# Performance work log

Hardware: AMD Instinct MI355X
Metric: run time of the kernel (lower is better)

## Reference

```python
import jax, jax.numpy as jnp
import numpy as np

B, N, E = 64, 512, 8192          # graphs, nodes per graph, edges per graph
F_IN, H, C = 128, 128, 10        # in features, hidden, classes
K1, K2 = 256, 128                # dense pool cluster counts: ceil(.5*N), ceil(.5*K1)
EPS = 1e-15


def setup_inputs():
    key = jax.random.key(0)
    keys = jax.random.split(key, 32)
    it = iter(keys)
    def w(shape, fan_in):
        return jax.random.normal(next(it), shape, jnp.float32) / np.sqrt(fan_in)
    x = jax.random.normal(next(it), (B * N, F_IN), jnp.float32)
    src_l = jax.random.randint(next(it), (B, E), 0, N)
    dst_l = jax.random.randint(next(it), (B, E), 0, N)
    off = (jnp.arange(B) * N)[:, None]
    src = (src_l + off).reshape(-1).astype(jnp.int32)
    dst = (dst_l + off).reshape(-1).astype(jnp.int32)
    return dict(
        x=x, src=src, dst=dst,
        conv0_wr=w((F_IN, H), F_IN), conv0_wroot=w((F_IN, H), F_IN), conv0_b=jnp.zeros((H,), jnp.float32),
        sconv2_wr=w((H, H), H), sconv2_wroot=w((H, H), H), sconv2_b=jnp.zeros((H,), jnp.float32),
        sconv3_wr=w((H, H), H), sconv3_wroot=w((H, H), H), sconv3_b=jnp.zeros((H,), jnp.float32),
        sage1_wr=w((H, H), H), sage1_wroot=w((H, H), H), sage1_b=jnp.zeros((H,), jnp.float32),
        sage2_wr=w((H, H), H), sage2_wroot=w((H, H), H), sage2_b=jnp.zeros((H,), jnp.float32),
        pool0_w=w((H, K1), H), pool0_b=jnp.zeros((K1,), jnp.float32),
        pool1_w=w((H, K2), H), pool1_b=jnp.zeros((K2,), jnp.float32),
        p1=w((H,), H), p2=w((H,), H), p3=w((H,), H),
        lin1_1_w=w((2 * H, H), 2 * H), lin1_1_b=jnp.zeros((H,), jnp.float32),
        lin1_w=w((H, H), H), lin1_b=jnp.zeros((H,), jnp.float32),
        lin2_w=w((2 * H, C), 2 * H), lin2_b=jnp.zeros((C,), jnp.float32),
    )


def _graph_conv(x, src, dst, emask, wr, wroot, b, n):
    # PyG GraphConv: lin_rel(sum_j x_j) + lin_root(x_i); invalid edges masked to 0.
    msg = x[src] * emask[:, None]
    agg = jax.ops.segment_sum(msg, dst, num_segments=n)
    return agg @ wr + x @ wroot + b


def _topk_pool(x, score_w, src, dst, emask, n_per_graph, k):
    # TopK pooling (MPoolS): score = x.w/||w||, keep top ratio*n per graph, gate by tanh(score).
    score = x @ score_w / (jnp.linalg.norm(score_w) + 1e-16)
    idx = jax.lax.top_k(score.reshape(B, n_per_graph), k)[1]
    perm = (idx + (jnp.arange(B) * n_per_graph)[:, None]).reshape(-1)
    new_x = x[perm] * jnp.tanh(score[perm])[:, None]
    new_id = jnp.full((B * n_per_graph,), -1, jnp.int32).at[perm].set(
        jnp.arange(B * k, dtype=jnp.int32))
    ns, nd = new_id[src], new_id[dst]
    valid = (ns >= 0) & (nd >= 0) & (emask > 0)
    return new_x, jnp.where(valid, ns, 0), jnp.where(valid, nd, 0), valid.astype(x.dtype)


def _readout(x, k):
    # gmp || gap per graph (nodes are contiguous, k per graph)
    xr = x.reshape(B, k, -1)
    return jnp.concatenate([xr.max(axis=1), xr.mean(axis=1)], axis=-1)


def _dense_sage(x, adj, wr, wroot, b):
    agg = (adj @ x) / jnp.clip(adj.sum(-1, keepdims=True), 1.0, None)
    return agg @ wr + x @ wroot + b


def _dense_mincut_pool(x, adj, s):
    s = jax.nn.softmax(s, axis=-1)
    k = s.shape[-1]
    out = jnp.einsum('bnk,bnf->bkf', s, x)
    out_adj = jnp.einsum('bnk,bnm,bml->bkl', s, adj, s)
    mincut_num = jnp.trace(out_adj, axis1=-2, axis2=-1)
    deg = adj.sum(-1)
    mincut_den = jnp.einsum('bn,bnk,bnk->b', deg, s, s)
    mc = -jnp.mean(mincut_num / (mincut_den + EPS))
    ss = jnp.einsum('bnk,bnl->bkl', s, s)
    ss_n = jnp.linalg.norm(ss, axis=(1, 2), keepdims=True)
    eye = jnp.eye(k, dtype=x.dtype)
    o = jnp.mean(jnp.linalg.norm(ss / (ss_n + EPS) - eye / jnp.sqrt(k), axis=(1, 2)))
    di = jnp.arange(k)
    out_adj = out_adj.at[:, di, di].set(0.0)
    dpool = jnp.sqrt(out_adj.sum(-1)) + EPS
    out_adj = out_adj / dpool[:, :, None] / dpool[:, None, :]
    return out, out_adj, mc, o


def _forward(x, src, dst, conv0_wr, conv0_wroot, conv0_b, sconv2_wr, sconv2_wroot, sconv2_b,
             sconv3_wr, sconv3_wroot, sconv3_b, sage1_wr, sage1_wroot, sage1_b,
             sage2_wr, sage2_wroot, sage2_b, pool0_w, pool0_b, pool1_w, pool1_b,
             p1, p2, p3, lin1_1_w, lin1_1_b, lin1_w, lin1_b, lin2_w, lin2_b):
    relu = jax.nn.relu
    e0 = jnp.ones((src.shape[0],), x.dtype)
    x0 = relu(_graph_conv(x, src, dst, e0, conv0_wr, conv0_wroot, conv0_b, B * N))
    # ---- sparse (MPoolS / top-k) branch, stage 1 ----
    sx, s1, d1, m1 = _topk_pool(x0, p1, src, dst, e0, N, N // 2)
    sx1 = _readout(sx, N // 2)
    # ---- dense (DiffPool-style) branch ----
    xd = x0.reshape(B, N, H)                               # to_dense_batch (full mask)
    g = src // N
    adj = jnp.zeros((B, N, N), x.dtype).at[g, src % N, dst % N].add(1.0)  # to_dense_adj
    s = xd @ pool0_w + pool0_b
    xd, adj, mc, o = _dense_mincut_pool(xd, adj, s)
    xd = relu(_dense_sage(xd, adj, sage1_wr, sage1_wroot, sage1_b))
    s = xd @ pool1_w + pool1_b
    xd, adj, mc2, o2 = _dense_mincut_pool(xd, adj, s)
    mc, o = mc + mc2, o + o2
    xd = _dense_sage(xd, adj, sage2_wr, sage2_wroot, sage2_b)
    xg = relu(xd.mean(axis=1) @ lin1_w + lin1_b)
    # ---- sparse branch, stages 2 and 3 ----
    sx = relu(_graph_conv(sx, s1, d1, m1, sconv2_wr, sconv2_wroot, sconv2_b, B * (N // 2)))
    sx, s2, d2, m2 = _topk_pool(sx, p2, s1, d1, m1, N // 2, N // 4)
    sx2 = _readout(sx, N // 4)
    sx = relu(_graph_conv(sx, s2, d2, m2, sconv3_wr, sconv3_wroot, sconv3_b, B * (N // 4)))
    sx, s3, d3, m3 = _topk_pool(sx, p3, s2, d2, m2, N // 4, N // 8)
    sx3 = _readout(sx, N // 8)
    sxr = relu((sx1 + sx2 + sx3) @ lin1_1_w + lin1_1_b)
    logits = jnp.concatenate([sxr, xg], axis=-1) @ lin2_w + lin2_b
    return logits, mc, o


def reference(x, src, dst, conv0_wr, conv0_wroot, conv0_b, sconv2_wr, sconv2_wroot, sconv2_b,
              sconv3_wr, sconv3_wroot, sconv3_b, sage1_wr, sage1_wroot, sage1_b,
              sage2_wr, sage2_wroot, sage2_b, pool0_w, pool0_b, pool1_w, pool1_b,
              p1, p2, p3, lin1_1_w, lin1_1_b, lin1_w, lin1_b, lin2_w, lin2_b):
    return _forward(x, src, dst, conv0_wr, conv0_wroot, conv0_b, sconv2_wr, sconv2_wroot,
                    sconv2_b, sconv3_wr, sconv3_wroot, sconv3_b, sage1_wr, sage1_wroot,
                    sage1_b, sage2_wr, sage2_wroot, sage2_b, pool0_w, pool0_b, pool1_w,
                    pool1_b, p1, p2, p3, lin1_1_w, lin1_1_b, lin1_w, lin1_b, lin2_w, lin2_b)
```

## Files before the change

### kernel.cpp

```cpp
#include <hip/hip_runtime.h>
#include <math.h>

#define NGRAPH 64
#define NE 524288
#define EPG 8192
#define TSZ 2560

typedef short s16x8 __attribute__((ext_vector_type(8)));
typedef float f32x4 __attribute__((ext_vector_type(4)));

__device__ inline unsigned short f2bf(float f) {
    unsigned int u = __float_as_uint(f);
    return (unsigned short)((u + 0x7FFFu + ((u >> 16) & 1u)) >> 16);
}
__device__ inline float bf2f(unsigned short h) {
    return __uint_as_float((unsigned int)h << 16);
}
__device__ inline unsigned int f2pk(float v) {
    unsigned short h = f2bf(v);
    return (unsigned int)h | ((unsigned int)f2bf(v - bf2f(h)) << 16);
}

__global__ void edge_count2(const int* __restrict__ keyA, int* __restrict__ cntA,
                            const int* __restrict__ keyB, int* __restrict__ cntB) {
    int e = blockIdx.x * 256 + threadIdx.x;
    if (e >= NE) return;
    if (blockIdx.y == 0) atomicAdd(&cntA[keyA[e]], 1);
    else                 atomicAdd(&cntB[keyB[e]], 1);
}

__device__ inline void scan_body(const int* __restrict__ counts, int* __restrict__ offs,
                                 int* __restrict__ cursor, int nPerGraph,
                                 float* __restrict__ degOut, int* s) {
    const int g = blockIdx.x, t = threadIdx.x;
    int v = (t < nPerGraph) ? counts[g * nPerGraph + t] : 0;
    s[t] = v; __syncthreads();
    for (int d = 1; d < 512; d <<= 1) {
        int u = (t >= d) ? s[t - d] : 0;
        __syncthreads();
        s[t] += u;
        __syncthreads();
    }
    if (t < nPerGraph) {
        int o = g * EPG + s[t] - v;
        offs[g * nPerGraph + t] = o;
        cursor[g * nPerGraph + t] = o;
        if (degOut) degOut[g * nPerGraph + t] = (float)v;
    }
}

__global__ __launch_bounds__(512) void scan_offsets(const int* __restrict__ counts,
        int* __restrict__ offs, int* __restrict__ cursor, int nPerGraph,
        float* __restrict__ degOut) {
    __shared__ int s[512];
    scan_body(counts, offs, cursor, nPerGraph, degOut, s);
}

__global__ __launch_bounds__(512) void scan_offsets2(
        const int* __restrict__ cA, int* __restrict__ oA, int* __restrict__ uA,
        const int* __restrict__ cB, int* __restrict__ oB, int* __restrict__ uB,
        int nPerGraph, float* __restrict__ degB) {
    __shared__ int s[512];
    if (blockIdx.y == 0) scan_body(cA, oA, uA, nPerGraph, nullptr, s);
    else                 scan_body(cB, oB, uB, nPerGraph, degB, s);
}

__global__ void edge_fill(const int* __restrict__ key, const int* __restrict__ payload,
                          const float* __restrict__ mask, int* __restrict__ cursor,
                          int* __restrict__ elist) {
    int e = blockIdx.x * 256 + threadIdx.x;
    if (e < NE && (!mask || mask[e] > 0.f)) {
        int p = atomicAdd(&cursor[key[e]], 1);
        elist[p] = payload[e];
    }
}

__global__ void edge_fill2(const int* __restrict__ kA, const int* __restrict__ pA,
                           int* __restrict__ uA, int* __restrict__ eA,
                           const int* __restrict__ kB, const int* __restrict__ pB,
                           int* __restrict__ uB, int* __restrict__ eB) {
    int e = blockIdx.x * 256 + threadIdx.x;
    if (e >= NE) return;
    if (blockIdx.y == 0) { int p = atomicAdd(&uA[kA[e]], 1); eA[p] = pA[e]; }
    else                 { int p = atomicAdd(&uB[kB[e]], 1); eB[p] = pB[e]; }
}

__device__ inline void addpk(float4& acc, uint4 u) {
    acc.x += __uint_as_float(u.x << 16) + __uint_as_float(u.x & 0xffff0000u);
    acc.y += __uint_as_float(u.y << 16) + __uint_as_float(u.y & 0xffff0000u);
    acc.z += __uint_as_float(u.z << 16) + __uint_as_float(u.z & 0xffff0000u);
    acc.w += __uint_as_float(u.w << 16) + __uint_as_float(u.w & 0xffff0000u);
}

__global__ __launch_bounds__(256) void gather_csr(
    const float* __restrict__ xf, const unsigned int* __restrict__ xp, int Fx,
    const int* __restrict__ offs, const int* __restrict__ cnts,
    const int* __restrict__ elist,
    unsigned int* __restrict__ opk,
    int totRows, int rowsPerGraph)
{
    const int gid = (blockIdx.x * 256 + threadIdx.x) >> 5;
    const int lane = threadIdx.x & 31;
    const int csh = (Fx == 256) ? 1 : 0;
    const int rid = gid >> csh;
    const int c0 = (gid & ((1 << csh) - 1)) << 7;
    if (rid >= totRows) return;
    const int row = (rid & 63) * rowsPerGraph + (rid >> 6);
    const int beg = offs[row];
    const int n = cnts[row];
    const long long co = (long long)c0 + (lane << 2);
    float4 acc = make_float4(0.f, 0.f, 0.f, 0.f);
    int j = 0;
    if (xp) {
        for (; j + 4 <= n; j += 4) {
            const int n0 = elist[beg + j], n1 = elist[beg + j + 1];
            const int n2 = elist[beg + j + 2], n3 = elist[beg + j + 3];
            const uint4 u0 = *(const uint4*)&xp[(long long)n0 * Fx + co];
            const uint4 u1 = *(const uint4*)&xp[(long long)n1 * Fx + co];
            const uint4 u2 = *(const uint4*)&xp[(long long)n2 * Fx + co];
            const uint4 u3 = *(const uint4*)&xp[(long long)n3 * Fx + co];
            addpk(acc, u0); addpk(acc, u1); addpk(acc, u2); addpk(acc, u3);
        }
        for (; j < n; ++j)
            addpk(acc, *(const uint4*)&xp[(long long)elist[beg + j] * Fx + co]);
    } else {
        for (; j + 4 <= n; j += 4) {
            const int n0 = elist[beg + j], n1 = elist[beg + j + 1];
            const int n2 = elist[beg + j + 2], n3 = elist[beg + j + 3];
            const float4 v0 = *(const float4*)&xf[(long long)n0 * Fx + co];
            const float4 v1 = *(const float4*)&xf[(long long)n1 * Fx + co];
            const float4 v2 = *(const float4*)&xf[(long long)n2 * Fx + co];
            const float4 v3 = *(const float4*)&xf[(long long)n3 * Fx + co];
            acc.x += v0.x + v1.x + v2.x + v3.x;
            acc.y += v0.y + v1.y + v2.y + v3.y;
            acc.z += v0.z + v1.z + v2.z + v3.z;
            acc.w += v0.w + v1.w + v2.w + v3.w;
        }
        for (; j < n; ++j) {
            const float4 v = *(const float4*)&xf[(long long)elist[beg + j] * Fx + co];
            acc.x += v.x; acc.y += v.y; acc.z += v.z; acc.w += v.w;
        }
    }
    uint4 pk;
    pk.x = f2pk(acc.x); pk.y = f2pk(acc.y); pk.z = f2pk(acc.z); pk.w = f2pk(acc.w);
    *(uint4*)&opk[(long long)row * Fx + co] = pk;
}

struct WSpec {
    const float* w1; const float* w2; int K1; int K2; int Nn;
    unsigned short* oh; unsigned short* ol;
};

__global__ void wconv_all(WSpec s0, WSpec s1, WSpec s2, WSpec s3, WSpec s4, WSpec s5, WSpec s6) {
    WSpec s;
    switch (blockIdx.y) {
        case 0: s = s0; break; case 1: s = s1; break; case 2: s = s2; break;
        case 3: s = s3; break; case 4: s = s4; break; case 5: s = s5; break;
        default: s = s6; break;
    }
    int idx = blockIdx.x * 256 + threadIdx.x;
    int Kt = s.K1 + s.K2;
    if (idx >= s.Nn * Kt) return;
    int n = idx / Kt, k = idx - n * Kt;
    float v = (k < s.K1) ? s.w1[(long long)k * s.Nn + n] : s.w2[(long long)(k - s.K1) * s.Nn + n];
    unsigned short h = f2bf(v);
    s.oh[idx] = h;
    s.ol[idx] = f2bf(v - __uint_as_float((unsigned int)h << 16));
}

__device__ inline void stageN_split(const float* __restrict__ src, int ldk, int k0,
                                    short* lds, int tid) {
    const int r = tid >> 2, kq = (tid & 3) << 3;
    const float* p = src + (long long)r * ldk + k0 + kq;
    float v[8];
    *(float4*)v = *(const float4*)p;
    *(float4*)(v + 4) = *(const float4*)(p + 4);
    s16x8 hv, lv;
    #pragma unroll
    for (int i = 0; i < 8; ++i) {
        unsigned short h = f2bf(v[i]);
        float hf = __uint_as_float((unsigned int)h << 16);
        hv[i] = (short)h;
        lv[i] = (short)f2bf(v[i] - hf);
    }
    *(s16x8*)(lds + r * 40 + kq) = hv;
    *(s16x8*)(lds + TSZ + r * 40 + kq) = lv;
}

__device__ inline void stageN_pk(const unsigned int* __restrict__ src, int ldk, int k0,
                                 short* lds, int tid) {
    const int r = tid >> 2, kq = (tid & 3) << 3;
    const unsigned int* p = src + (long long)r * ldk + k0 + kq;
    uint4 a = *(const uint4*)p;
    uint4 b = *(const uint4*)(p + 4);
    uint4 hw, lw;
    hw.x = (a.x & 0xffffu) | (a.y << 16);
    hw.y = (a.z & 0xffffu) | (a.w << 16);
    hw.z = (b.x & 0xffffu) | (b.y << 16);
    hw.w = (b.z & 0xffffu) | (b.w << 16);
    lw.x = (a.x >> 16) | (a.y & 0xffff0000u);
    lw.y = (a.z >> 16) | (a.w & 0xffff0000u);
    lw.z = (b.x >> 16) | (b.y & 0xffff0000u);
    lw.w = (b.z >> 16) | (b.w & 0xffff0000u);
    *(uint4*)(lds + r * 40 + kq) = hw;
    *(uint4*)(lds + TSZ + r * 40 + kq) = lw;
}

__device__ inline void stageT_pk(const unsigned int* __restrict__ P,
                                 int ldm, int k0, int m0, short* lds, int tid) {
    const int kp = tid >> 4, mc = tid & 15;
    const int k = kp << 1;
    const unsigned int* p0 = P + (long long)(k0 + k) * ldm + m0 + mc;
    const unsigned int* p1 = p0 + ldm;
    #pragma unroll
    for (int i = 0; i < 4; ++i) {
        unsigned int e0 = p0[i << 4], e1 = p1[i << 4];
        const int o = (mc + (i << 4)) * 40 + k;
        *(unsigned int*)(lds + o) = (e0 & 0xffffu) | (e1 << 16);
        *(unsigned int*)(lds + o + TSZ) = (e0 >> 16) | (e1 & 0xffff0000u);
    }
}

__device__ inline void stageW_split(const unsigned short* __restrict__ wh,
                                    const unsigned short* __restrict__ wl, int ldk,
                                    int n0, int k0, short* lds, int tid) {
    const int r = tid >> 2, kq = (tid & 3) << 3;
    *(s16x8*)(lds + r * 40 + kq) = *(const s16x8*)(wh + (long long)(n0 + r) * ldk + k0 + kq);
    *(s16x8*)(lds + TSZ + r * 40 + kq) = *(const s16x8*)(wl + (long long)(n0 + r) * ldk + k0 + kq);
}

__device__ inline void loadT8(const unsigned int* __restrict__ P, int ldm, int k0, int m0,
                              int tid, unsigned int (&r)[8]) {
    const int kp = tid >> 4, mc = tid & 15;
    const int k = kp << 1;
    const unsigned int* p0 = P + (long long)(k0 + k) * ldm + m0 + mc;
    const unsigned int* p1 = p0 + ldm;
    #pragma unroll
    for (int i = 0; i < 4; ++i) { r[i] = p0[i << 4]; r[4 + i] = p1[i << 4]; }
}
__device__ inline void storeT8(short* lds, int tid, const unsigned int (&r)[8]) {
    const int kp = tid >> 4, mc = tid & 15;
    const int k = kp << 1;
    #pragma unroll
    for (int i = 0; i < 4; ++i) {
        unsigned int e0 = r[i], e1 = r[4 + i];
        const int o = (mc + (i << 4)) * 40 + k;
        *(unsigned int*)(lds + o) = (e0 & 0xffffu) | (e1 << 16);
        *(unsigned int*)(lds + o + TSZ) = (e0 >> 16) | (e1 & 0xffff0000u);
    }
}
__device__ inline void storeT8_hi(short* lds, int tid, const unsigned int (&r)[8]) {
    const int kp = tid >> 4, mc = tid & 15;
    const int k = kp << 1;
    #pragma unroll
    for (int i = 0; i < 4; ++i)
        *(unsigned int*)(lds + (mc + (i << 4)) * 40 + k) =
            (r[i] & 0xffffu) | (r[4 + i] << 16);
}

__device__ inline void mfma_split(const short* As, const short* Bs, int wm, int wn,
                                  int l15, int quad, f32x4 (&acc)[2][2]) {
    const int ko = quad << 3;
    s16x8 ah[2], al[2], bh[2], bl[2];
    #pragma unroll
    for (int i = 0; i < 2; ++i) {
        const int ra = (wm + (i << 4) + l15) * 40 + ko;
        const int rb = (wn + (i << 4) + l15) * 40 + ko;
        ah[i] = *(const s16x8*)&As[ra];
        al[i] = *(const s16x8*)&As[TSZ + ra];
        bh[i] = *(const s16x8*)&Bs[rb];
        bl[i] = *(const s16x8*)&Bs[TSZ + rb];
    }
    #pragma unroll
    for (int mi = 0; mi < 2; ++mi)
    #pragma unroll
    for (int ni = 0; ni < 2; ++ni) {
        f32x4 c = acc[mi][ni];
        c = __builtin_amdgcn_mfma_f32_16x16x32_bf16(ah[mi], bh[ni], c, 0, 0, 0);
        c = __builtin_amdgcn_mfma_f32_16x16x32_bf16(ah[mi], bl[ni], c, 0, 0, 0);
        c = __builtin_amdgcn_mfma_f32_16x16x32_bf16(al[mi], bh[ni], c, 0, 0, 0);
        acc[mi][ni] = c;
    }
}

__device__ inline void mfma_hi(const short* As, const short* Bs, int wm, int wn,
                               int l15, int quad, f32x4 (&acc)[2][2]) {
    const int ko = quad << 3;
    s16x8 ah[2], bh[2];
    #pragma unroll
    for (int i = 0; i < 2; ++i) {
        ah[i] = *(const s16x8*)&As[(wm + (i << 4) + l15) * 40 + ko];
        bh[i] = *(const s16x8*)&Bs[(wn + (i << 4) + l15) * 40 + ko];
    }
    #pragma unroll
    for (int mi = 0; mi < 2; ++mi)
    #pragma unroll
    for (int ni = 0; ni < 2; ++ni)
        acc[mi][ni] = __builtin_amdgcn_mfma_f32_16x16x32_bf16(ah[mi], bh[ni], acc[mi][ni], 0, 0, 0);
}

__global__ __launch_bounds__(256) void gemm_aw(
    const unsigned int* __restrict__ A1p, const float* __restrict__ A1f, int K1,
    const unsigned int* __restrict__ A2p, const float* __restrict__ A2f, int K2,
    const unsigned short* __restrict__ Wh, const unsigned short* __restrict__ Wl,
    const float* __restrict__ bias, float* __restrict__ C,
    unsigned int* __restrict__ Cpk,
    int Nn, int doRelu)
{
    __shared__ short As[2 * TSZ], Bs[2 * TSZ];
    const int m0 = blockIdx.y << 6, n0 = blockIdx.x << 6;
    const int tid = threadIdx.x, lane = tid & 63, wv = tid >> 6;
    const int l15 = lane & 15, quad = lane >> 4;
    const int wm = (wv & 1) << 5, wn = (wv >> 1) << 5;
    f32x4 acc[2][2] = {};
    const int Kt = K1 + K2;
    for (int k0 = 0; k0 < Kt; k0 += 32) {
        if (k0 < K1) {
            if (A1p) stageN_pk(A1p + (long long)m0 * K1, K1, k0, As, tid);
            else     stageN_split(A1f + (long long)m0 * K1, K1, k0, As, tid);
        } else {
            if (A2p) stageN_pk(A2p + (long long)m0 * K2, K2, k0 - K1, As, tid);
            else     stageN_split(A2f + (long long)m0 * K2, K2, k0 - K1, As, tid);
        }
        stageW_split(Wh, Wl, Kt, n0, k0, Bs, tid);
        __syncthreads();
        mfma_split(As, Bs, wm, wn, l15, quad, acc);
        __syncthreads();
    }
    #pragma unroll
    for (int mi = 0; mi < 2; ++mi)
    #pragma unroll
    for (int ni = 0; ni < 2; ++ni) {
        const int col = n0 + wn + (ni << 4) + l15;
        const float bv = bias ? bias[col] : 0.f;
        #pragma unroll
        for (int r = 0; r < 4; ++r) {
            const int row = m0 + wm + (mi << 4) + (quad << 2) + r;
            float v = acc[mi][ni][r] + bv;
            if (doRelu) v = fmaxf(v, 0.f);
            if (C)   C[(long long)row * Nn + col] = v;
            if (Cpk) Cpk[(long long)row * Nn + col] = f2pk(v);
        }
    }
}

struct TTSet {
    const unsigned int* Bp;
    float* C; unsigned int* Cpk; float* fro;
    int Nn; int dual;
    long long sB, sC;
    float* rsum; float* rdiag;
};

__global__ __launch_bounds__(256) void gemm_tt(
    const unsigned int* __restrict__ Ap, int Kd, int Mm, long long sA,
    int zsplit, TTSet t0, TTSet t1)
{
    __shared__ short As[2 * TSZ], Bs[2 * TSZ], A2s[TSZ];
    __shared__ float redf[4];
    const int z = blockIdx.x;
    int nz = blockIdx.z;
    const TTSet tt = (nz < zsplit) ? t0 : t1;
    if (blockIdx.z >= zsplit) nz -= zsplit;
    const unsigned int* Apz = Ap + (long long)z * sA;
    const unsigned int* Bpz = tt.Bp + (long long)z * tt.sB;
    const int m0 = blockIdx.y << 6, n0 = nz << 6;
    const int tid = threadIdx.x, lane = tid & 63, wv = tid >> 6;
    const int l15 = lane & 15, quad = lane >> 4;
    const int wm = (wv & 1) << 5, wn = (wv >> 1) << 5;
    const int fw = tt.dual ? ((m0 < n0) ? 2 : ((m0 == n0) ? 1 : 0)) : 0;
    f32x4 acc[2][2] = {};
    f32x4 accA[2][2] = {};
    unsigned int ra[8], rb[8], rh[8];
    loadT8(Apz, Mm, 0, m0, tid, ra);
    loadT8(Bpz, tt.Nn, 0, n0, tid, rb);
    if (fw) loadT8(Apz, Mm, 0, n0, tid, rh);
    for (int k0 = 0; k0 < Kd; k0 += 32) {
        storeT8(As, tid, ra);
        storeT8(Bs, tid, rb);
        if (fw) storeT8_hi(A2s, tid, rh);
        __syncthreads();
        const int kn = k0 + 32;
        if (kn < Kd) {
            loadT8(Apz, Mm, kn, m0, tid, ra);
            loadT8(Bpz, tt.Nn, kn, n0, tid, rb);
            if (fw) loadT8(Apz, Mm, kn, n0, tid, rh);
        }
        mfma_split(As, Bs, wm, wn, l15, quad, acc);
        if (fw) mfma_hi(As, A2s, wm, wn, l15, quad, accA);
        __syncthreads();
    }
    float* Cp = tt.C ? tt.C + (long long)z * tt.sC : nullptr;
    unsigned int* Ckp = tt.Cpk ? tt.Cpk + (long long)z * tt.sC : nullptr;
    #pragma unroll
    for (int mi = 0; mi < 2; ++mi)
    #pragma unroll
    for (int ni = 0; ni < 2; ++ni) {
        const int col = n0 + wn + (ni << 4) + l15;
        #pragma unroll
        for (int r = 0; r < 4; ++r) {
            const int row = m0 + wm + (mi << 4) + (quad << 2) + r;
            const float v = acc[mi][ni][r];
            if (Cp)  Cp[(long long)row * tt.Nn + col] = v;
            if (Ckp) Ckp[(long long)row * tt.Nn + col] = f2pk(v);
        }
    }
    if (tt.rsum) {
        #pragma unroll
        for (int mi = 0; mi < 2; ++mi) {
            #pragma unroll
            for (int r = 0; r < 4; ++r) {
                float rs = acc[mi][0][r] + acc[mi][1][r];
                rs += __shfl_xor(rs, 1);
                rs += __shfl_xor(rs, 2);
                rs += __shfl_xor(rs, 4);
                rs += __shfl_xor(rs, 8);
                if (l15 == 0) {
                    const int row = m0 + wm + (mi << 4) + (quad << 2) + r;
                    atomicAdd(&tt.rsum[z * tt.Nn + row], rs);
                }
            }
        }
        if (tt.rdiag && m0 == n0) {
            #pragma unroll
            for (int mi = 0; mi < 2; ++mi)
            #pragma unroll
            for (int ni = 0; ni < 2; ++ni)
            #pragma unroll
            for (int r = 0; r < 4; ++r) {
                const int rr = wm + (mi << 4) + (quad << 2) + r;
                const int cc = wn + (ni << 4) + l15;
                if (rr == cc) tt.rdiag[z * tt.Nn + m0 + rr] = acc[mi][ni][r];
            }
        }
    }
    if (fw) {
        float s = 0.f;
        #pragma unroll
        for (int mi = 0; mi < 2; ++mi)
        #pragma unroll
        for (int ni = 0; ni < 2; ++ni)
        #pragma unroll
        for (int r = 0; r < 4; ++r) s += accA[mi][ni][r] * accA[mi][ni][r];
        s *= (float)fw;
        for (int off = 32; off; off >>= 1) s += __shfl_xor(s, off);
        if (lane == 0) redf[wv] = s;
        __syncthreads();
        if (tid == 0) atomicAdd(&tt.fro[z], redf[0] + redf[1] + redf[2] + redf[3]);
    }
}

__global__ __launch_bounds__(256) void gemm_nt(
    const unsigned short* __restrict__ Ah, const unsigned short* __restrict__ Al,
    const unsigned int* __restrict__ Bp,
    float* __restrict__ C, unsigned int* __restrict__ Cpk,
    const float* __restrict__ rscale, int rsn,
    int Kd, int Nn, long long sA, long long sB, long long sC)
{
    __shared__ short As[2 * TSZ], Bs[2 * TSZ];
    const int z = blockIdx.x;
    const int m0 = blockIdx.y << 6, n0 = blockIdx.z << 6;
    const unsigned short* Aph = Ah + (long long)z * sA;
    const unsigned short* Apl = Al + (long long)z * sA;
    const unsigned int* Bpz = Bp + (long long)z * sB;
    const int tid = threadIdx.x, lane = tid & 63, wv = tid >> 6;
    const int l15 = lane & 15, quad = lane >> 4;
    const int wm = (wv & 1) << 5, wn = (wv >> 1) << 5;
    f32x4 acc[2][2] = {};
    unsigned int rb[8];
    loadT8(Bpz, Nn, 0, n0, tid, rb);
    for (int k0 = 0; k0 < Kd; k0 += 32) {
        stageW_split(Aph, Apl, Kd, m0, k0, As, tid);
        storeT8(Bs, tid, rb);
        __syncthreads();
        const int kn = k0 + 32;
        if (kn < Kd) loadT8(Bpz, Nn, kn, n0, tid, rb);
        mfma_split(As, Bs, wm, wn, l15, quad, acc);
        __syncthreads();
    }
    #pragma unroll
    for (int mi = 0; mi < 2; ++mi)
    #pragma unroll
    for (int ni = 0; ni < 2; ++ni) {
        const int col = n0 + wn + (ni << 4) + l15;
        #pragma unroll
        for (int r = 0; r < 4; ++r) {
            const int row = m0 + wm + (mi << 4) + (quad << 2) + r;
            float v = acc[mi][ni][r];
            if (rscale) v *= rscale[z * rsn + row];
            if (C)   C[(long long)z * sC + (long long)row * Nn + col] = v;
            if (Cpk) Cpk[(long long)z * sC + (long long)row * Nn + col] = f2pk(v);
        }
    }
}

__global__ __launch_bounds__(256) void softmax_rows_wave(
    const float* __restrict__ sm, int L,
    const float* __restrict__ deg,
    float* __restrict__ rowq2, float* __restrict__ rowdq2, int totRows,
    unsigned int* __restrict__ opk)
{
    const int wid = (blockIdx.x * 256 + threadIdx.x) >> 6;
    const int lane = threadIdx.x & 63;
    if (wid >= totRows) return;
    const float* rowp = sm + (long long)wid * L;
    const int nv = L >> 6;
    float v[4];
    if (nv == 4) {
        float4 t = *(const float4*)&rowp[lane << 2];
        v[0] = t.x; v[1] = t.y; v[2] = t.z; v[3] = t.w;
    } else {
        float2 t = *(const float2*)&rowp[lane << 1];
        v[0] = t.x; v[1] = t.y;
    }
    float mx = v[0];
    for (int i = 1; i < nv; ++i) mx = fmaxf(mx, v[i]);
    for (int off = 32; off; off >>= 1) mx = fmaxf(mx, __shfl_xor(mx, off));
    float s = 0.f;
    for (int i = 0; i < nv; ++i) { v[i] = expf(v[i] - mx); s += v[i]; }
    for (int off = 32; off; off >>= 1) s += __shfl_xor(s, off);
    const float inv = 1.f / s;
    float q2 = 0.f;
    for (int i = 0; i < nv; ++i) { float p = v[i] * inv; v[i] = p; q2 += p * p; }
    const long long rb = (long long)wid * L;
    if (nv == 4) {
        uint4 pk;
        pk.x = f2pk(v[0]); pk.y = f2pk(v[1]); pk.z = f2pk(v[2]); pk.w = f2pk(v[3]);
        *(uint4*)&opk[rb + (lane << 2)] = pk;
    } else {
        uint2 pk;
        pk.x = f2pk(v[0]); pk.y = f2pk(v[1]);
        *(uint2*)&opk[rb + (lane << 1)] = pk;
    }
    for (int off = 32; off; off >>= 1) q2 += __shfl_xor(q2, off);
    if (lane == 0) { rowq2[wid] = q2; rowdq2[wid] = deg[wid] * q2; }
}

__global__ __launch_bounds__(256) void reduce2_pergraph(
    const float* __restrict__ a, const float* __restrict__ b, int rowsPerGraph,
    float* __restrict__ outA, float* __restrict__ outB)
{
    __shared__ float redA[4], redB[4];
    const int g = blockIdx.x, t = threadIdx.x;
    float sa = 0.f, sb = 0.f;
    for (int i = t; i < rowsPerGraph; i += 256) {
        sa += a[g * rowsPerGraph + i];
        if (b) sb += b[g * rowsPerGraph + i];
    }
    for (int off = 32; off; off >>= 1) { sa += __shfl_xor(sa, off); sb += __shfl_xor(sb, off); }
    const int wv = t >> 6;
    if ((t & 63) == 0) { redA[wv] = sa; redB[wv] = sb; }
    __syncthreads();
    if (t == 0) {
        outA[g] = redA[0] + redA[1] + redA[2] + redA[3];
        if (outB) outB[g] = redB[0] + redB[1] + redB[2] + redB[3];
    }
}

__global__ __launch_bounds__(1024) void adjnorm(
    const float* __restrict__ adj, int K,
    const float* __restrict__ rsumIn, const float* __restrict__ rdiagIn,
    float* __restrict__ trace_out,
    float* __restrict__ rowsum, float* __restrict__ rscale,
    unsigned short* __restrict__ oh, unsigned short* __restrict__ ol)
{
    __shared__ float dpoolL[256];
    __shared__ float redt[16];
    const int g = blockIdx.x, tid = threadIdx.x;
    const int wv = tid >> 6, lane = tid & 63;
    float trp = 0.f;
    for (int r = tid; r < K; r += 1024) {
        float dv = rdiagIn[g * K + r];
        dpoolL[r] = sqrtf(rsumIn[g * K + r] - dv) + 1e-15f;
        trp += dv;
    }
    for (int off = 32; off; off >>= 1) trp += __shfl_xor(trp, off);
    if (lane == 0) redt[wv] = trp;
    __syncthreads();
    if (tid == 0) {
        float t = 0.f;
        #pragma unroll
        for (int i = 0; i < 16; ++i) t += redt[i];
        trace_out[g] = t;
    }
    const int rowsPerWave = K >> 4;
    const int nv = K >> 6;
    for (int rr = 0; rr < rowsPerWave; ++rr) {
        const int r = wv * rowsPerWave + rr;
        const int wid = g * K + r;
        const float* rowp = adj + (long long)wid * K;
        const float inv_r = 1.f / dpoolL[r];
        float s = 0.f;
        for (int q = 0; q < nv; ++q) {
            int c = lane + (q << 6);
            float a = rowp[c];
            if (c == r) a = 0.f;
            float v = a * inv_r / dpoolL[c];
            s += v;
            unsigned short h = f2bf(v);
            oh[(long long)wid * K + c] = h;
            ol[(long long)wid * K + c] = f2bf(v - bf2f(h));
        }
        for (int off = 32; off; off >>= 1) s += __shfl_xor(s, off);
        if (lane == 0) { rowsum[wid] = s; rscale[wid] = 1.f / fmaxf(s, 1.f); }
    }
}

__global__ __launch_bounds__(512) void topk_fused(
    const float* __restrict__ x, const float* __restrict__ p, int n, int k,
    int* __restrict__ new_id, float* __restrict__ outx,
    float* __restrict__ sxsum, int* __restrict__ cntZero)
{
    __shared__ float sc[512];
    __shared__ int pref[512];
    __shared__ int   selL[256];
    __shared__ float gateL[256];
    __shared__ float red[1024];
    const int g = blockIdx.x, tid = threadIdx.x;
    if (cntZero && tid < k) cntZero[g * k + tid] = 0;
    float myScore = 0.f;
    if (tid < n) {
        const float* xr = x + (long long)(g * n + tid) * 128;
        float pn2 = 0.f, d = 0.f;
        #pragma unroll 4
        for (int f = 0; f < 128; f += 4) {
            float4 pv = *(const float4*)&p[f];
            float4 v = *(const float4*)&xr[f];
            pn2 += pv.x * pv.x + pv.y * pv.y + pv.z * pv.z + pv.w * pv.w;
            d += v.x * pv.x + v.y * pv.y + v.z * pv.z + v.w * pv.w;
        }
        myScore = d / (sqrtf(pn2) + 1e-16f);
        sc[tid] = myScore;
    }
    __syncthreads();
    int keep = 0;
    if (tid < n) {
        const float si = myScore;
        int rank = 0;
        for (int j = 0; j < n; j += 4) {
            float4 s4 = *(const float4*)&sc[j];
            rank += (s4.x > si) || (s4.x == si && (j + 0) < tid);
            rank += (s4.y > si) || (s4.y == si && (j + 1) < tid);
            rank += (s4.z > si) || (s4.z == si && (j + 2) < tid);
            rank += (s4.w > si) || (s4.w == si && (j + 3) < tid);
        }
        keep = rank < k;
    }
    pref[tid] = keep;
    __syncthreads();
    for (int d = 1; d < 512; d <<= 1) {
        int u = (tid >= d) ? pref[tid - d] : 0;
        __syncthreads();
        pref[tid] += u;
        __syncthreads();
    }
    if (tid < n) {
        if (keep) {
            int pos = pref[tid] - 1;
            new_id[g * n + tid] = g * k + pos;
            selL[pos] = g * n + tid;
            gateL[pos] = tanhf(myScore);
        } else new_id[g * n + tid] = -1;
    }
    __syncthreads();
    const int f = tid & 127, grp = tid >> 7;
    float mx = -INFINITY, sm = 0.f;
    for (int r = grp; r < k; r += 4) {
        float v = x[(long long)selL[r] * 128 + f] * gateL[r];
        outx[(long long)(g * k + r) * 128 + f] = v;
        mx = fmaxf(mx, v); sm += v;
    }
    red[grp * 128 + f] = mx;
    red[512 + grp * 128 + f] = sm;
    __syncthreads();
    if (tid < 128) {
        float m = fmaxf(fmaxf(red[f], red[128 + f]), fmaxf(red[256 + f], red[384 + f]));
        float s2 = red[512 + f] + red[640 + f] + red[768 + f] + red[896 + f];
        sxsum[g * 256 + f] += m;
        sxsum[g * 256 + 128 + f] += s2 / k;
    }
}

__global__ void remap_edges_count(const int* __restrict__ s, const int* __restrict__ d,
                                  const float* __restrict__ m, const int* __restrict__ new_id,
                                  int* __restrict__ so, int* __restrict__ do_,
                                  float* __restrict__ mo, int* __restrict__ counts) {
    int e = blockIdx.x * blockDim.x + threadIdx.x;
    if (e >= NE) return;
    int ns = new_id[s[e]], nd = new_id[d[e]];
    bool v = (ns >= 0) && (nd >= 0) && (m ? (m[e] > 0.f) : true);
    so[e] = v ? ns : 0; do_[e] = v ? nd : 0; mo[e] = v ? 1.f : 0.f;
    if (v) atomicAdd(&counts[nd], 1);
}

__global__ void final_head(const float* __restrict__ sxsum, const float* __restrict__ w11,
                           const float* __restrict__ b11,
                           const float* __restrict__ xd2, const float* __restrict__ l1w,
                           const float* __restrict__ l1b,
                           const float* __restrict__ w2, const float* __restrict__ b2,
                           const float* __restrict__ accs, float* __restrict__ out) {
    __shared__ float meanv[128];
    __shared__ float sin_[256];
    __shared__ float cat[256];
    __shared__ float rm[2], ro[2];
    int b = blockIdx.x, t = threadIdx.x;
    {
        float s = 0.f;
        for (int n = 0; n < 128; n++) s += xd2[(long long)(b * 128 + n) * 128 + t];
        meanv[t] = s / 128.f;
    }
    if (b == 0) {
        int wvi = t >> 6, lane = t & 63;
        const float* acc = accs + wvi * 256;
        float sqrtk = wvi ? sqrtf(128.f) : 16.f;
        float numv = acc[lane], denv = acc[64 + lane], trv = acc[128 + lane], frov = acc[192 + lane];
        float mcb = numv / (denv + 1e-15f);
        float ssn = sqrtf(frov) + 1e-15f;
        float ob = sqrtf(fmaxf(frov / (ssn * ssn) - 2.f * trv / (ssn * sqrtk) + 1.f, 0.f));
        for (int off = 32; off; off >>= 1) { mcb += __shfl_down(mcb, off); ob += __shfl_down(ob, off); }
        if (lane == 0) { rm[wvi] = mcb; ro[wvi] = ob; }
        __syncthreads();
        if (t == 0) {
            out[640] = -(rm[0] + rm[1]) / 64.f;
            out[641] = (ro[0] + ro[1]) / 64.f;
        }
    }
    sin_[t] = sxsum[b * 256 + t];
    sin_[t + 128] = sxsum[b * 256 + 128 + t];
    __syncthreads();
    float acc = b11[t];
    for (int i = 0; i < 256; i++) acc += sin_[i] * w11[i * 128 + t];
    cat[t] = fmaxf(acc, 0.f);
    float xga = l1b[t];
    for (int i = 0; i < 128; i++) xga += meanv[i] * l1w[i * 128 + t];
    cat[128 + t] = fmaxf(xga, 0.f);
    __syncthreads();
    if (t < 10) {
        float a = b2[t];
        for (int i = 0; i < 256; i++) a += cat[i] * w2[i * 10 + t];
        out[b * 10 + t] = a;
    }
}

extern "C" void kernel_launch(void* const* d_in, const int* in_sizes, int n_in,
                              void* d_out, int out_size, void* d_ws, size_t ws_size,
                              hipStream_t stream) {
    const float* x         = (const float*)d_in[0];
    const int*   src       = (const int*)d_in[1];
    const int*   dst       = (const int*)d_in[2];
    const float* conv0_wr  = (const float*)d_in[3];
    const float* conv0_wrt = (const float*)d_in[4];
    const float* conv0_b   = (const float*)d_in[5];
    const float* sc2_wr    = (const float*)d_in[6];
    const float* sc2_wrt   = (const float*)d_in[7];
    const float* sc2_b     = (const float*)d_in[8];
    const float* sc3_wr    = (const float*)d_in[9];
    const float* sc3_wrt   = (const float*)d_in[10];
    const float* sc3_b     = (const float*)d_in[11];
    const float* sg1_wr    = (const float*)d_in[12];
    const float* sg1_wrt   = (const float*)d_in[13];
    const float* sg1_b     = (const float*)d_in[14];
    const float* sg2_wr    = (const float*)d_in[15];
    const float* sg2_wrt   = (const float*)d_in[16];
    const float* sg2_b     = (const float*)d_in[17];
    const float* pool0_w   = (const float*)d_in[18];
    const float* pool0_b   = (const float*)d_in[19];
    const float* pool1_w   = (const float*)d_in[20];
    const float* pool1_b   = (const float*)d_in[21];
    const float* p1        = (const float*)d_in[22];
    const float* p2        = (const float*)d_in[23];
    const float* p3        = (const float*)d_in[24];
    const float* l11_w     = (const float*)d_in[25];
    const float* l11_b     = (const float*)d_in[26];
    const float* l1_w      = (const float*)d_in[27];
    const float* l1_b      = (const float*)d_in[28];
    const float* l2_w      = (const float*)d_in[29];
    const float* l2_b      = (const float*)d_in[30];
    float* out = (float*)d_out;

    char* w = (char*)d_ws;
    const unsigned long long MBy = 1ull << 20;
    float* x0    = (float*)(w + 0);
    float* BIG1  = (float*)(w + 16 * MBy);
    float* BIG2  = (float*)(w + 48 * MBy);
    float* agg   = (float*)(w + 80 * MBy);
    float* adj1  = (float*)(w + 104 * MBy);
    int*   s1    = (int*)(w + 120 * MBy);
    int*   d1    = (int*)(w + 122 * MBy);
    float* m1    = (float*)(w + 124 * MBy);
    int*   s2e   = (int*)(w + 126 * MBy);
    int*   d2e   = (int*)(w + 128 * MBy);
    float* m2e   = (float*)(w + 130 * MBy);
    char*  misc  = w + 132 * MBy;
    float* rowq2  = (float*)(misc);
    float* rowdq2 = (float*)(misc + 128 * 1024);
    int*   newid = (int*)(misc + 256 * 1024);
    float* deg   = (float*)(misc + 384 * 1024);
    float* rowsum2 = (float*)(misc + 576 * 1024);
    float* rscale2 = (float*)(misc + 640 * 1024);
    float* rowsum3 = (float*)(misc + 736 * 1024);
    float* rscale3 = (float*)(misc + 768 * 1024);
    float* accs    = (float*)(misc + 800 * 1024);
    float* sxsum   = (float*)(misc + 900 * 1024);

    unsigned short* wt_sg1h   = (unsigned short*)(misc + 1024 * 1024);
    unsigned short* wt_sg1l   = wt_sg1h + 32768;
    unsigned short* wt_sg2h   = wt_sg1l + 32768;
    unsigned short* wt_sg2l   = wt_sg2h + 32768;
    unsigned short* wt_pool0h = wt_sg2l + 32768;
    unsigned short* wt_pool0l = wt_pool0h + 32768;
    unsigned short* wt_pool1h = wt_pool0l + 32768;
    unsigned short* wt_pool1l = wt_pool1h + 32768;
    unsigned short* wt_c0h    = wt_pool1l + 32768;
    unsigned short* wt_c0l    = wt_c0h + 32768;
    unsigned short* wt_sc2h   = wt_c0l + 32768;
    unsigned short* wt_sc2l   = wt_sc2h + 32768;
    unsigned short* wt_sc3h   = wt_sc2l + 32768;
    unsigned short* wt_sc3l   = wt_sc3h + 32768;

    float* rsum1  = (float*)(misc + 2048 * 1024);
    float* rdiag1 = (float*)(misc + 2112 * 1024);
    float* rsum2  = (float*)(misc + 2176 * 1024);
    float* rdiag2 = (float*)(misc + 2208 * 1024);

    float* s_sm  = BIG1;
    unsigned int* Tbp = (unsigned int*)BIG2;
    float* s2sm  = BIG2 + 4 * 1024 * 1024;
    unsigned int* T2p = (unsigned int*)((char*)BIG2 + 24 * MBy);
    float* adj2b = BIG1 + 1024 * 1024;
    float* xd2   = BIG1 + 2 * 1024 * 1024;
    float* sxA   = BIG1 + 3 * 1024 * 1024;
    float* sxE   = BIG1 + 5 * 1024 * 1024;
    float* sxB   = x0;
    float* sxC   = x0 + 2 * 1024 * 1024;
    float* sxD   = x0 + 3 * 1024 * 1024;

    unsigned int* s_smp = (unsigned int*)(w + 136 * MBy);
    unsigned int* x0p   = (unsigned int*)(w + 168 * MBy);
    unsigned int* ox1p  = (unsigned int*)(w + 184 * MBy);
    unsigned int* xd1p  = (unsigned int*)(w + 192 * MBy);
    unsigned int* s2p   = (unsigned int*)(w + 200 * MBy);
    unsigned int* ox2p  = (unsigned int*)(w + 208 * MBy);
    unsigned short* a1h = (unsigned short*)(w + 212 * MBy);
    unsigned short* a1l = (unsigned short*)(w + 220 * MBy);
    unsigned short* a2h = (unsigned short*)(w + 228 * MBy);
    unsigned short* a2l = (unsigned short*)(w + 230 * MBy);
    unsigned int* AXp   = (unsigned int*)(w + 232 * MBy);
    unsigned int* AXp2  = (unsigned int*)(w + 240 * MBy);

    unsigned int* aggp  = (unsigned int*)agg;
    unsigned int* agg2p = (unsigned int*)agg;
    unsigned int* agg3p = (unsigned int*)agg;

    char* adjc = (char*)adj1;
    int* elA  = (int*)(adjc + 0);
    int* elB  = (int*)(adjc + 2 * MBy);
    int* cntA = (int*)(adjc + 4 * MBy);
    int* cntB = (int*)(adjc + 4 * MBy + 128 * 1024);
    int* offA = (int*)(adjc + 4 * MBy + 256 * 1024);
    int* curA = (int*)(adjc + 4 * MBy + 384 * 1024);
    int* offB = (int*)(adjc + 4 * MBy + 512 * 1024);
    int* curB = (int*)(adjc + 4 * MBy + 640 * 1024);
    char* aggc = (char*)agg;
    int* elC  = (int*)(aggc + 8 * MBy);
    int* elD  = (int*)(aggc + 10 * MBy);
    int* cntC = (int*)(aggc + 12 * MBy);
    int* offC = (int*)(aggc + 12 * MBy + 256 * 1024);
    int* curC = (int*)(aggc + 12 * MBy + 512 * 1024);
    int* cntD = (int*)(aggc + 13 * MBy);
    int* offD = (int*)(aggc + 13 * MBy + 256 * 1024);
    int* curD = (int*)(aggc + 13 * MBy + 512 * 1024);

    hipMemsetAsync(accs, 0, 520 * sizeof(float), stream);
    hipMemsetAsync(sxsum, 0, 16384 * sizeof(float), stream);
    hipMemsetAsync(cntA, 0, 65536 * sizeof(int), stream);
    hipMemsetAsync(rsum1, 0, 128 * 1024, stream);
    hipMemsetAsync(rsum2, 0, 64 * 1024, stream);

    {
        WSpec a{sg1_wr, sg1_wrt, 128, 128, 128, wt_sg1h, wt_sg1l};
        WSpec b{sg2_wr, sg2_wrt, 128, 128, 128, wt_sg2h, wt_sg2l};
        WSpec c{pool0_w, nullptr, 128, 0, 256, wt_pool0h, wt_pool0l};
        WSpec d{pool1_w, nullptr, 128, 0, 128, wt_pool1h, wt_pool1l};
        WSpec e{conv0_wr, conv0_wrt, 128, 128, 128, wt_c0h, wt_c0l};
        WSpec f{sc2_wr, sc2_wrt, 128, 128, 128, wt_sc2h, wt_sc2l};
        WSpec g{sc3_wr, sc3_wrt, 128, 128, 128, wt_sc3h, wt_sc3l};
        wconv_all<<<dim3(128, 7), 256, 0, stream>>>(a, b, c, d, e, f, g);
    }

    edge_count2<<<dim3(2048, 2), 256, 0, stream>>>(dst, cntA, src, cntB);
    scan_offsets2<<<dim3(64, 2), 512, 0, stream>>>(cntA, offA, curA, cntB, offB, curB, 512, deg);
    edge_fill2<<<dim3(2048, 2), 256, 0, stream>>>(dst, src, curA, elA, src, dst, curB, elB);

    gather_csr<<<4096, 256, 0, stream>>>(x, nullptr, 128, offA, cntA, elA, aggp, 32768, 512);
    gemm_aw<<<dim3(2, 512), 256, 0, stream>>>(aggp, nullptr, 128, nullptr, x, 128,
        wt_c0h, wt_c0l, conv0_b, x0, x0p, 128, 1);

    gemm_aw<<<dim3(4, 512), 256, 0, stream>>>(x0p, nullptr, 128, nullptr, nullptr, 0,
        wt_pool0h, wt_pool0l, pool0_b, s_sm, nullptr, 256, 0);
    softmax_rows_wave<<<8192, 256, 0, stream>>>(s_sm, 256, deg, rowq2, rowdq2, 32768, s_smp);
    reduce2_pergraph<<<64, 256, 0, stream>>>(rowq2, rowdq2, 512, accs + 128, accs + 64);
    gather_csr<<<8192, 256, 0, stream>>>(nullptr, s_smp, 256, offB, cntB, elB, Tbp, 32768, 512);
    {
        TTSet t0{x0p, nullptr, ox1p, nullptr, 128, 0, 512 * 128, 256 * 128, nullptr, nullptr};
        TTSet t1{Tbp, adj1, nullptr, accs + 192, 256, 1, 512 * 256, 256 * 256, rsum1, rdiag1};
        gemm_tt<<<dim3(64, 4, 6), 256, 0, stream>>>(s_smp, 512, 256, 512 * 256, 2, t0, t1);
    }
    adjnorm<<<64, 1024, 0, stream>>>(adj1, 256, rsum1, rdiag1, accs + 0,
        rowsum2, rscale2, a1h, a1l);
    gemm_nt<<<dim3(64, 4, 2), 256, 0, stream>>>(a1h, a1l, ox1p, nullptr, AXp, rscale2, 256,
        256, 128, 256 * 256, 256 * 128, 256 * 128);
    gemm_aw<<<dim3(2, 256), 256, 0, stream>>>(AXp, nullptr, 128, ox1p, nullptr, 128,
        wt_sg1h, wt_sg1l, sg1_b, nullptr, xd1p, 128, 1);
    gemm_aw<<<dim3(2, 256), 256, 0, stream>>>(xd1p, nullptr, 128, nullptr, nullptr, 0,
        wt_pool1h, wt_pool1l, pool1_b, s2sm, nullptr, 128, 0);
    softmax_rows_wave<<<4096, 256, 0, stream>>>(s2sm, 128, rowsum2, rowq2, rowdq2, 16384, s2p);
    reduce2_pergraph<<<64, 256, 0, stream>>>(rowq2, rowdq2, 256, accs + 384, accs + 320);
    gemm_nt<<<dim3(64, 4, 2), 256, 0, stream>>>(a1h, a1l, s2p, nullptr, T2p, nullptr, 0,
        256, 128, 256 * 256, 256 * 128, 256 * 128);
    {
        TTSet t0{xd1p, nullptr, ox2p, nullptr, 128, 0, 256 * 128, 128 * 128, nullptr, nullptr};
        TTSet t1{T2p, adj2b, nullptr, accs + 448, 128, 1, 256 * 128, 128 * 128, rsum2, rdiag2};
        gemm_tt<<<dim3(64, 2, 4), 256, 0, stream>>>(s2p, 256, 128, 256 * 128, 2, t0, t1);
    }
    adjnorm<<<64, 1024, 0, stream>>>(adj2b, 128, rsum2, rdiag2, accs + 256,
        rowsum3, rscale3, a2h, a2l);
    gemm_nt<<<dim3(64, 2, 2), 256, 0, stream>>>(a2h, a2l, ox2p, nullptr, AXp2, rscale3, 128,
        128, 128, 128 * 128, 128 * 128, 128 * 128);
    gemm_aw<<<dim3(2, 128), 256, 0, stream>>>(AXp2, nullptr, 128, ox2p, nullptr, 128,
        wt_sg2h, wt_sg2l, sg2_b, xd2, nullptr, 128, 0);

    topk_fused<<<64, 512, 0, stream>>>(x0, p1, 512, 256, newid, sxA, sxsum, cntC);
    remap_edges_count<<<2048, 256, 0, stream>>>(src, dst, nullptr, newid, s1, d1, m1, cntC);
    scan_offsets<<<64, 512, 0, stream>>>(cntC, offC, curC, 256, nullptr);
    edge_fill<<<2048, 256, 0, stream>>>(d1, s1, m1, curC, elC);
    gather_csr<<<2048, 256, 0, stream>>>(sxA, nullptr, 128, offC, cntC, elC, agg2p, 16384, 256);
    gemm_aw<<<dim3(2, 256), 256, 0, stream>>>(agg2p, nullptr, 128, nullptr, sxA, 128,
        wt_sc2h, wt_sc2l, sc2_b, sxB, nullptr, 128, 1);
    topk_fused<<<64, 512, 0, stream>>>(sxB, p2, 256, 128, newid, sxC, sxsum, cntD);
    remap_edges_count<<<2048, 256, 0, stream>>>(s1, d1, m1, newid, s2e, d2e, m2e, cntD);
    scan_offsets<<<64, 512, 0, stream>>>(cntD, offD, curD, 128, nullptr);
    edge_fill<<<2048, 256, 0, stream>>>(d2e, s2e, m2e, curD, elD);
    gather_csr<<<1024, 256, 0, stream>>>(sxC, nullptr, 128, offD, cntD, elD, agg3p, 8192, 128);
    gemm_aw<<<dim3(2, 128), 256, 0, stream>>>(agg3p, nullptr, 128, nullptr, sxC, 128,
        wt_sc3h, wt_sc3l, sc3_b, sxD, nullptr, 128, 1);
    topk_fused<<<64, 512, 0, stream>>>(sxD, p3, 128, 64, newid, sxE, sxsum, nullptr);

    final_head<<<64, 128, 0, stream>>>(sxsum, l11_w, l11_b, xd2, l1_w, l1_b,
        l2_w, l2_b, accs, out);
}
```

Measured before the change: 629.2 us.

## Fuse edge remap, count, scan and CSR fill into per-graph topk kernel

The top-k pooling kernel now also remaps each graph's edges with a shared-memory new-id table, counts in-degrees with shared atomics, scans the counts into offsets and fills the CSR edge list. This replaces three separate launches (remap_edges_count, scan_offsets, edge_fill) per pooling stage and the global newid and cursor buffers. In exchange each of the 64 blocks walks its 8192 edges twice on its own, so this phase runs on only 64 workgroups where the removed kernels used 2048.

Result: no change. 626.9 us (-0.4%).

```diff
diff --git a/kernel.cpp b/kernel.cpp
--- a/kernel.cpp
+++ b/kernel.cpp
@@ -49,13 +49,6 @@
     }
 }
 
-__global__ __launch_bounds__(512) void scan_offsets(const int* __restrict__ counts,
-        int* __restrict__ offs, int* __restrict__ cursor, int nPerGraph,
-        float* __restrict__ degOut) {
-    __shared__ int s[512];
-    scan_body(counts, offs, cursor, nPerGraph, degOut, s);
-}
-
 __global__ __launch_bounds__(512) void scan_offsets2(
         const int* __restrict__ cA, int* __restrict__ oA, int* __restrict__ uA,
         const int* __restrict__ cB, int* __restrict__ oB, int* __restrict__ uB,
@@ -63,16 +56,6 @@
     __shared__ int s[512];
     if (blockIdx.y == 0) scan_body(cA, oA, uA, nPerGraph, nullptr, s);
     else                 scan_body(cB, oB, uB, nPerGraph, degB, s);
-}
-
-__global__ void edge_fill(const int* __restrict__ key, const int* __restrict__ payload,
-                          const float* __restrict__ mask, int* __restrict__ cursor,
-                          int* __restrict__ elist) {
-    int e = blockIdx.x * 256 + threadIdx.x;
-    if (e < NE && (!mask || mask[e] > 0.f)) {
-        int p = atomicAdd(&cursor[key[e]], 1);
-        elist[p] = payload[e];
-    }
 }
 
 __global__ void edge_fill2(const int* __restrict__ kA, const int* __restrict__ pA,
@@ -608,16 +591,20 @@
 
 __global__ __launch_bounds__(512) void topk_fused(
     const float* __restrict__ x, const float* __restrict__ p, int n, int k,
-    int* __restrict__ new_id, float* __restrict__ outx,
-    float* __restrict__ sxsum, int* __restrict__ cntZero)
+    float* __restrict__ outx, float* __restrict__ sxsum,
+    const int* __restrict__ sIn, const int* __restrict__ dIn, const float* __restrict__ mIn,
+    int* __restrict__ sOut, int* __restrict__ dOut, float* __restrict__ mOut,
+    int* __restrict__ elist, int* __restrict__ offs, int* __restrict__ cnts)
 {
     __shared__ float sc[512];
     __shared__ int pref[512];
     __shared__ int   selL[256];
     __shared__ float gateL[256];
     __shared__ float red[1024];
+    __shared__ int   nidL[512];
+    __shared__ int   cntL[256];
+    __shared__ int   curL[256];
     const int g = blockIdx.x, tid = threadIdx.x;
-    if (cntZero && tid < k) cntZero[g * k + tid] = 0;
     float myScore = 0.f;
     if (tid < n) {
         const float* xr = x + (long long)(g * n + tid) * 128;
@@ -654,13 +641,15 @@
         pref[tid] += u;
         __syncthreads();
     }
-    if (tid < n) {
-        if (keep) {
+    {
+        int nid = -1;
+        if (tid < n && keep) {
             int pos = pref[tid] - 1;
-            new_id[g * n + tid] = g * k + pos;
+            nid = g * k + pos;
             selL[pos] = g * n + tid;
             gateL[pos] = tanhf(myScore);
-        } else new_id[g * n + tid] = -1;
+        }
+        nidL[tid] = nid;
     }
     __syncthreads();
     const int f = tid & 127, grp = tid >> 7;
@@ -679,18 +668,53 @@
         sxsum[g * 256 + f] += m;
         sxsum[g * 256 + 128 + f] += s2 / k;
     }
-}
-
-__global__ void remap_edges_count(const int* __restrict__ s, const int* __restrict__ d,
-                                  const float* __restrict__ m, const int* __restrict__ new_id,
-                                  int* __restrict__ so, int* __restrict__ do_,
-                                  float* __restrict__ mo, int* __restrict__ counts) {
-    int e = blockIdx.x * blockDim.x + threadIdx.x;
-    if (e >= NE) return;
-    int ns = new_id[s[e]], nd = new_id[d[e]];
-    bool v = (ns >= 0) && (nd >= 0) && (m ? (m[e] > 0.f) : true);
-    so[e] = v ? ns : 0; do_[e] = v ? nd : 0; mo[e] = v ? 1.f : 0.f;
-    if (v) atomicAdd(&counts[nd], 1);
+    if (sIn) {
+        if (tid < k) cntL[tid] = 0;
+        __syncthreads();
+        const int e0 = g * EPG;
+        for (int e = e0 + tid; e < e0 + EPG; e += 512) {
+            bool vin = mIn ? (mIn[e] > 0.f) : true;
+            int ns = -1, nd = -1;
+            if (vin) {
+                ns = nidL[sIn[e] - g * n];
+                nd = nidL[dIn[e] - g * n];
+            }
+            bool v = (ns >= 0) && (nd >= 0);
+            sOut[e] = v ? ns : 0;
+            dOut[e] = v ? nd : 0;
+            mOut[e] = v ? 1.f : 0.f;
+            if (v) atomicAdd(&cntL[nd - g * k], 1);
+        }
+        __syncthreads();
+        int c = (tid < k) ? cntL[tid] : 0;
+        pref[tid] = c;
+        __syncthreads();
+        for (int d = 1; d < 512; d <<= 1) {
+            int u = (tid >= d) ? pref[tid - d] : 0;
+            __syncthreads();
+            pref[tid] += u;
+            __syncthreads();
+        }
+        if (tid < k) {
+            int o = pref[tid] - c;
+            offs[g * k + tid] = e0 + o;
+            cnts[g * k + tid] = c;
+            curL[tid] = o;
+        }
+        __syncthreads();
+        for (int e = e0 + tid; e < e0 + EPG; e += 512) {
+            bool vin = mIn ? (mIn[e] > 0.f) : true;
+            int ns = -1, nd = -1;
+            if (vin) {
+                ns = nidL[sIn[e] - g * n];
+                nd = nidL[dIn[e] - g * n];
+            }
+            if (ns >= 0 && nd >= 0) {
+                int p_ = atomicAdd(&curL[nd - g * k], 1);
+                elist[e0 + p_] = ns;
+            }
+        }
+    }
 }
 
 __global__ void final_head(const float* __restrict__ sxsum, const float* __restrict__ w11,
@@ -794,7 +818,6 @@
     char*  misc  = w + 132 * MBy;
     float* rowq2  = (float*)(misc);
     float* rowdq2 = (float*)(misc + 128 * 1024);
-    int*   newid = (int*)(misc + 256 * 1024);
     float* deg   = (float*)(misc + 384 * 1024);
     float* rowsum2 = (float*)(misc + 576 * 1024);
     float* rscale2 = (float*)(misc + 640 * 1024);
@@ -866,10 +889,8 @@
     int* elD  = (int*)(aggc + 10 * MBy);
     int* cntC = (int*)(aggc + 12 * MBy);
     int* offC = (int*)(aggc + 12 * MBy + 256 * 1024);
-    int* curC = (int*)(aggc + 12 * MBy + 512 * 1024);
     int* cntD = (int*)(aggc + 13 * MBy);
     int* offD = (int*)(aggc + 13 * MBy + 256 * 1024);
-    int* curD = (int*)(aggc + 13 * MBy + 512 * 1024);
 
     hipMemsetAsync(accs, 0, 520 * sizeof(float), stream);
     hipMemsetAsync(sxsum, 0, 16384 * sizeof(float), stream);
@@ -930,21 +951,18 @@
     gemm_aw<<<dim3(2, 128), 256, 0, stream>>>(AXp2, nullptr, 128, ox2p, nullptr, 128,
         wt_sg2h, wt_sg2l, sg2_b, xd2, nullptr, 128, 0);
 
-    topk_fused<<<64, 512, 0, stream>>>(x0, p1, 512, 256, newid, sxA, sxsum, cntC);
-    remap_edges_count<<<2048, 256, 0, stream>>>(src, dst, nullptr, newid, s1, d1, m1, cntC);
-    scan_offsets<<<64, 512, 0, stream>>>(cntC, offC, curC, 256, nullptr);
-    edge_fill<<<2048, 256, 0, stream>>>(d1, s1, m1, curC, elC);
+    topk_fused<<<64, 512, 0, stream>>>(x0, p1, 512, 256, sxA, sxsum,
+        src, dst, nullptr, s1, d1, m1, elC, offC, cntC);
     gather_csr<<<2048, 256, 0, stream>>>(sxA, nullptr, 128, offC, cntC, elC, agg2p, 16384, 256);
     gemm_aw<<<dim3(2, 256), 256, 0, stream>>>(agg2p, nullptr, 128, nullptr, sxA, 128,
         wt_sc2h, wt_sc2l, sc2_b, sxB, nullptr, 128, 1);
-    topk_fused<<<64, 512, 0, stream>>>(sxB, p2, 256, 128, newid, sxC, sxsum, cntD);
-    remap_edges_count<<<2048, 256, 0, stream>>>(s1, d1, m1, newid, s2e, d2e, m2e, cntD);
-    scan_offsets<<<64, 512, 0, stream>>>(cntD, offD, curD, 128, nullptr);
-    edge_fill<<<2048, 256, 0, stream>>>(d2e, s2e, m2e, curD, elD);
+    topk_fused<<<64, 512, 0, stream>>>(sxB, p2, 256, 128, sxC, sxsum,
+        s1, d1, m1, s2e, d2e, m2e, elD, offD, cntD);
     gather_csr<<<1024, 256, 0, stream>>>(sxC, nullptr, 128, offD, cntD, elD, agg3p, 8192, 128);
     gemm_aw<<<dim3(2, 128), 256, 0, stream>>>(agg3p, nullptr, 128, nullptr, sxC, 128,
         wt_sc3h, wt_sc3l, sc3_b, sxD, nullptr, 128, 1);
-    topk_fused<<<64, 512, 0, stream>>>(sxD, p3, 128, 64, newid, sxE, sxsum, nullptr);
+    topk_fused<<<64, 512, 0, stream>>>(sxD, p3, 128, 64, sxE, sxsum,
+        nullptr, nullptr, nullptr, nullptr, nullptr, nullptr, nullptr, nullptr, nullptr);
 
     final_head<<<64, 128, 0, stream>>>(sxsum, l11_w, l11_b, xd2, l1_w, l1_b,
         l2_w, l2_b, accs, out);
```
